# Kernel optimization log

Hardware: AMD Instinct MI355X
Metric: run time of the kernel (lower is better)

## Reference

```python
import jax, jax.numpy as jnp
import numpy as np

B, T, E, H = 8, 2048, 1024, 64

def setup_inputs() -> dict:
    key = jax.random.key(0)
    ks = jax.random.split(key, 7)
    s = 1.0 / np.sqrt(E)
    return {
        "x": jax.random.normal(ks[0], (B, T, E), dtype=jnp.float32),
        "Wq": jax.random.uniform(ks[1], (E, H), jnp.float32, -s, s),
        "bq": jax.random.uniform(ks[2], (H,), jnp.float32, -s, s),
        "Wk": jax.random.uniform(ks[3], (E, H), jnp.float32, -s, s),
        "bk": jax.random.uniform(ks[4], (H,), jnp.float32, -s, s),
        "Wv": jax.random.uniform(ks[5], (E, H), jnp.float32, -s, s),
        "bv": jax.random.uniform(ks[6], (H,), jnp.float32, -s, s),
        "mask": jnp.ones((B, T), dtype=jnp.int32),
    }

def reference(x, Wq, bq, Wk, bk, Wv, bv, mask):
    # QKV projections: [B,T,E] @ [E,H] -> [B,T,H]
    q = x @ Wq + bq
    k = x @ Wk + bk
    v = x @ Wv + bv
    scale = jnp.asarray(H, x.dtype) ** -0.5
    attn = jnp.einsum("bqh,bkh->bqk", q, k) * scale  # [B,T,T]
    pad = mask.astype(bool)[:, None, :]  # key padding mask broadcast over queries
    attn = jnp.where(pad, attn, jnp.asarray(-1e9, attn.dtype))
    attn = jax.nn.softmax(attn, axis=-1)
    # dropout p=0.0 (eval) -> identity
    return jnp.einsum("bqk,bkh->bqh", attn, v)
```

## Files before the change

kernel.cpp:

```cpp
#include <hip/hip_runtime.h>
#include <hip/hip_bf16.h>
#include <stdint.h>


typedef __attribute__((ext_vector_type(8))) short short8;
typedef __attribute__((ext_vector_type(4))) float floatx4;
typedef __attribute__((ext_vector_type(2))) uint32_t uint2v;
typedef __attribute__((ext_vector_type(4))) uint32_t uint4v;

static constexpr int Tn = 2048, En = 1024, Hn = 64;
static constexpr float kLog2e = 1.44269504088896340736f;

static __device__ __forceinline__ ushort f2bf(float f) {
  uint32_t u = __builtin_bit_cast(uint32_t, f);
  u += 0x7FFFu + ((u >> 16) & 1u);
  return (ushort)(u >> 16);
}
static __device__ __forceinline__ uint32_t cvt_pk(float lo, float hi) {
  uint32_t r;
  asm("v_cvt_pk_bf16_f32 %0, %1, %2" : "=v"(r) : "v"(lo), "v"(hi));
  return r;
}

__global__ __launch_bounds__(64) void k_packw(const float* __restrict__ Wq,
                                              const float* __restrict__ Wk,
                                              const float* __restrict__ Wv,
                                              ushort* __restrict__ wpack) {
  int blk = blockIdx.x;
  int kstep = blk / 12, ntile = blk % 12;
  int l = threadIdx.x;
  const float* W = (ntile < 4) ? Wq : (ntile < 8) ? Wk : Wv;
  int col = (ntile & 3) * 16 + (l & 15);
  int k0 = kstep * 32 + (l >> 4) * 8;
  short8 v;
#pragma unroll
  for (int j = 0; j < 8; ++j) v[j] = (short)f2bf(W[(k0 + j) * Hn + col]);
  *reinterpret_cast<short8*>(wpack + ((size_t)(kstep * 12 + ntile) * 64 + l) * 8) = v;
}

__global__ __launch_bounds__(256) void k_qkv(const float* __restrict__ x,
                                             const ushort* __restrict__ wpack,
                                             const float* __restrict__ bq,
                                             const float* __restrict__ bk,
                                             const float* __restrict__ bv,
                                             ushort* __restrict__ q,
                                             ushort* __restrict__ k,
                                             ushort* __restrict__ vT2) {
  __shared__ ushort xs[16][1032];
  int tid = threadIdx.x;
  int batch = blockIdx.x & 7;
  int chunk = blockIdx.x >> 3;
  int row0 = batch * Tn + chunk * 16;

  {
    const float* src = x + (size_t)row0 * En + tid * 4;
#pragma unroll
    for (int i = 0; i < 16; ++i) {
      floatx4 f = *reinterpret_cast<const floatx4*>(src + (size_t)i * En);
      uint2v u;
      u[0] = cvt_pk(f[0], f[1]);
      u[1] = cvt_pk(f[2], f[3]);
      *reinterpret_cast<uint2v*>(&xs[i][tid * 4]) = u;
    }
  }
  __syncthreads();

  int l = tid & 63;
  int w = tid >> 6;
  int lq = l & 15, g = l >> 4;
  const ushort* wpn = wpack + (((size_t)w * 3) * 64 + l) * 8;

  floatx4 acc[3];
#pragma unroll
  for (int nn = 0; nn < 3; ++nn) acc[nn] = (floatx4){0.f, 0.f, 0.f, 0.f};

#pragma unroll 4
  for (int ks = 0; ks < 32; ++ks) {
    short8 af = *reinterpret_cast<const short8*>(&xs[lq][ks * 32 + g * 8]);
#pragma unroll
    for (int nn = 0; nn < 3; ++nn) {
      short8 bf = *reinterpret_cast<const short8*>(wpn + (size_t)ks * 6144 + nn * 512);
      acc[nn] = __builtin_amdgcn_mfma_f32_16x16x32_bf16(af, bf, acc[nn], 0, 0, 0);
    }
  }

#pragma unroll
  for (int nn = 0; nn < 3; ++nn) {
    int n = w * 3 + nn;
    int mat = n >> 2;
    int h = (n & 3) * 16 + lq;
    const float* bias = (mat == 0) ? bq : (mat == 1) ? bk : bv;
    float bias_f = bias[h];
    if (mat == 0) {
#pragma unroll
      for (int r = 0; r < 4; ++r)
        q[(size_t)(row0 + g * 4 + r) * Hn + h] = f2bf((acc[nn][r] + bias_f) * 0.125f);
    } else if (mat == 1) {
#pragma unroll
      for (int r = 0; r < 4; ++r)
        k[(size_t)(row0 + g * 4 + r) * Hn + h] = f2bf(acc[nn][r] + bias_f);
    } else {
      int tile = chunk >> 1;
      int off = (chunk & 1) * 16 + g * 4;
      uint2v pk;
      pk[0] = cvt_pk(acc[nn][0] + bias_f, acc[nn][1] + bias_f);
      pk[1] = cvt_pk(acc[nn][2] + bias_f, acc[nn][3] + bias_f);
      *reinterpret_cast<uint2v*>(vT2 + (((size_t)batch * 64 + tile) * 64 + h) * 32 + off) = pk;
    }
  }
}

__global__ __launch_bounds__(512, 4) void k_attn(const ushort* __restrict__ qm,
                                                 const ushort* __restrict__ km,
                                                 const ushort* __restrict__ vT2,
                                                 const int* __restrict__ mask,
                                                 float* __restrict__ out) {
  __shared__ union SMem {
    ushort P[8][32 * 40];
    struct {
      float accS[4][64][36];
      float mS[4][2][64];
      float lS[4][2][64];
    } mg;
  } sm;

  int tid = threadIdx.x;
  int l = tid & 63, w = tid >> 6;
  int s = w;
  int bid = blockIdx.x;
  int b = bid & 7;
  int chunk = bid >> 3;
  int q0 = chunk * 32;
  int lq = l & 15, g = l >> 4;

  short8 qf[2][2];
#pragma unroll
  for (int qt2 = 0; qt2 < 2; ++qt2) {
    const ushort* qb = qm + ((size_t)(b * Tn + q0 + qt2 * 16 + lq)) * Hn + g * 8;
    qf[qt2][0] = *reinterpret_cast<const short8*>(qb);
    qf[qt2][1] = *reinterpret_cast<const short8*>(qb + 32);
  }

  const ushort* kp = km + ((size_t)(b * Tn + s * 256) + lq) * Hn + g * 8;
  const ushort* vp = vT2 + (((size_t)b * 64 + s * 8) * 64 + lq) * 32 + g * 8;

  const int* mrow = mask + b * Tn + s * 256 + l;
  unsigned long long bal64[4];
#pragma unroll
  for (int j = 0; j < 4; ++j) bal64[j] = __ballot(mrow[j * 64] != 0);

  ushort* Pw = &sm.P[w][0];
  uint32_t* Pw32 = reinterpret_cast<uint32_t*>(Pw);

  float m[2] = {-1e30f, -1e30f};
  float lsum[2] = {0.f, 0.f};
  floatx4 acc[2][4];
#pragma unroll
  for (int qt2 = 0; qt2 < 2; ++qt2)
#pragma unroll
    for (int mt = 0; mt < 4; ++mt) acc[qt2][mt] = (floatx4){0.f, 0.f, 0.f, 0.f};

  short8 kf[2][4];
#pragma unroll
  for (int t = 0; t < 2; ++t)
#pragma unroll
    for (int h = 0; h < 2; ++h)
      kf[0][t * 2 + h] = *reinterpret_cast<const short8*>(kp + t * 1024 + h * 32);

#pragma unroll
  for (int it = 0; it < 8; ++it) {
    const int cur = it & 1, nxt = cur ^ 1;
    if (it < 7) {
#pragma unroll
      for (int t = 0; t < 2; ++t)
#pragma unroll
        for (int h = 0; h < 2; ++h)
          kf[nxt][t * 2 + h] =
              *reinterpret_cast<const short8*>(kp + (it + 1) * 2048 + t * 1024 + h * 32);
    }
    short8 vf[4];
#pragma unroll
    for (int mt = 0; mt < 4; ++mt)
      vf[mt] = *reinterpret_cast<const short8*>(vp + it * 2048 + mt * 512);

    float sc[2][2][4];
#pragma unroll
    for (int qt2 = 0; qt2 < 2; ++qt2)
#pragma unroll
      for (int t = 0; t < 2; ++t) {
        floatx4 z = (floatx4){0.f, 0.f, 0.f, 0.f};
        z = __builtin_amdgcn_mfma_f32_16x16x32_bf16(kf[cur][t * 2 + 0], qf[qt2][0], z, 0, 0, 0);
        z = __builtin_amdgcn_mfma_f32_16x16x32_bf16(kf[cur][t * 2 + 1], qf[qt2][1], z, 0, 0, 0);
#pragma unroll
        for (int r = 0; r < 4; ++r) sc[qt2][t][r] = z[r];
      }
    unsigned int bal32 = (unsigned int)(bal64[it >> 1] >> ((it & 1) * 32));
    if (bal32 != 0xFFFFFFFFu) {
#pragma unroll
      for (int qt2 = 0; qt2 < 2; ++qt2)
#pragma unroll
        for (int t = 0; t < 2; ++t)
#pragma unroll
          for (int r = 0; r < 4; ++r)
            if (!((bal32 >> (t * 16 + g * 4 + r)) & 1u)) sc[qt2][t][r] = -1e9f;
    }
    float pmax0 = fmaxf(fmaxf(fmaxf(sc[0][0][0], sc[0][0][1]), fmaxf(sc[0][0][2], sc[0][0][3])),
                        fmaxf(fmaxf(sc[0][1][0], sc[0][1][1]), fmaxf(sc[0][1][2], sc[0][1][3])));
    float pmax1 = fmaxf(fmaxf(fmaxf(sc[1][0][0], sc[1][0][1]), fmaxf(sc[1][0][2], sc[1][0][3])),
                        fmaxf(fmaxf(sc[1][1][0], sc[1][1][1]), fmaxf(sc[1][1][2], sc[1][1][3])));
    if (!__all((pmax0 - m[0] <= 8.0f) && (pmax1 - m[1] <= 8.0f))) {
      float rm0 = fmaxf(pmax0, __shfl_xor(pmax0, 16));
      rm0 = fmaxf(rm0, __shfl_xor(rm0, 32));
      float rm1 = fmaxf(pmax1, __shfl_xor(pmax1, 16));
      rm1 = fmaxf(rm1, __shfl_xor(rm1, 32));
      float mn0 = fmaxf(m[0], rm0), mn1 = fmaxf(m[1], rm1);
      float a0 = __builtin_amdgcn_exp2f((m[0] - mn0) * kLog2e);
      float a1 = __builtin_amdgcn_exp2f((m[1] - mn1) * kLog2e);
      lsum[0] *= a0; lsum[1] *= a1;
#pragma unroll
      for (int mt = 0; mt < 4; ++mt) { acc[0][mt] *= a0; acc[1][mt] *= a1; }
      m[0] = mn0; m[1] = mn1;
    }
#pragma unroll
    for (int qt2 = 0; qt2 < 2; ++qt2) {
      float nmk = m[qt2] * kLog2e;
      float p[8];
#pragma unroll
      for (int t = 0; t < 2; ++t)
#pragma unroll
        for (int r = 0; r < 4; ++r)
          p[t * 4 + r] = __builtin_amdgcn_exp2f(__builtin_fmaf(sc[qt2][t][r], kLog2e, -nmk));
      lsum[qt2] += ((p[0] + p[1]) + (p[2] + p[3])) + ((p[4] + p[5]) + (p[6] + p[7]));
      uint2v pw0, pw1;
      pw0[0] = cvt_pk(p[0], p[1]); pw0[1] = cvt_pk(p[2], p[3]);
      pw1[0] = cvt_pk(p[4], p[5]); pw1[1] = cvt_pk(p[6], p[7]);
      int row = qt2 * 16 + lq;
      *reinterpret_cast<uint2v*>(Pw32 + row * 20 + g * 2) = pw0;
      *reinterpret_cast<uint2v*>(Pw32 + row * 20 + 8 + g * 2) = pw1;
    }
    short8 pf0 = *reinterpret_cast<const short8*>(Pw + (0 * 16 + lq) * 40 + g * 8);
    short8 pf1 = *reinterpret_cast<const short8*>(Pw + (1 * 16 + lq) * 40 + g * 8);
#pragma unroll
    for (int mt = 0; mt < 4; ++mt) {
      acc[0][mt] = __builtin_amdgcn_mfma_f32_16x16x32_bf16(vf[mt], pf0, acc[0][mt], 0, 0, 0);
      acc[1][mt] = __builtin_amdgcn_mfma_f32_16x16x32_bf16(vf[mt], pf1, acc[1][mt], 0, 0, 0);
    }
  }

#pragma unroll
  for (int qt2 = 0; qt2 < 2; ++qt2) {
    lsum[qt2] += __shfl_xor(lsum[qt2], 16);
    lsum[qt2] += __shfl_xor(lsum[qt2], 32);
  }

  __syncthreads();
  if (s >= 4) {
#pragma unroll
    for (int qt2 = 0; qt2 < 2; ++qt2) {
#pragma unroll
      for (int mt = 0; mt < 4; ++mt)
        *reinterpret_cast<floatx4*>(&sm.mg.accS[s - 4][l][qt2 * 16 + mt * 4]) = acc[qt2][mt];
      sm.mg.mS[s - 4][qt2][l] = m[qt2];
      sm.mg.lS[s - 4][qt2][l] = lsum[qt2];
    }
  }
  __syncthreads();
  if (s < 4) {
#pragma unroll
    for (int qt2 = 0; qt2 < 2; ++qt2) {
      float m2 = sm.mg.mS[s][qt2][l], l2 = sm.mg.lS[s][qt2][l];
      float mn = fmaxf(m[qt2], m2);
      float ea = __builtin_amdgcn_exp2f((m[qt2] - mn) * kLog2e);
      float eb = __builtin_amdgcn_exp2f((m2 - mn) * kLog2e);
      lsum[qt2] = lsum[qt2] * ea + l2 * eb;
#pragma unroll
      for (int mt = 0; mt < 4; ++mt) {
        floatx4 a = *reinterpret_cast<const floatx4*>(&sm.mg.accS[s][l][qt2 * 16 + mt * 4]);
#pragma unroll
        for (int r = 0; r < 4; ++r) acc[qt2][mt][r] = acc[qt2][mt][r] * ea + a[r] * eb;
      }
      m[qt2] = mn;
    }
  }
  __syncthreads();
  if (s >= 1 && s < 4) {
#pragma unroll
    for (int qt2 = 0; qt2 < 2; ++qt2) {
#pragma unroll
      for (int mt = 0; mt < 4; ++mt)
        *reinterpret_cast<floatx4*>(&sm.mg.accS[s - 1][l][qt2 * 16 + mt * 4]) = acc[qt2][mt];
      sm.mg.mS[s - 1][qt2][l] = m[qt2];
      sm.mg.lS[s - 1][qt2][l] = lsum[qt2];
    }
  }
  __syncthreads();
  if (s == 0) {
#pragma unroll
    for (int qt2 = 0; qt2 < 2; ++qt2) {
      float mtot = m[qt2];
#pragma unroll
      for (int si = 0; si < 3; ++si) mtot = fmaxf(mtot, sm.mg.mS[si][qt2][l]);
      float e0 = __builtin_amdgcn_exp2f((m[qt2] - mtot) * kLog2e);
      float ltot = lsum[qt2] * e0;
      float res[4][4];
#pragma unroll
      for (int mt = 0; mt < 4; ++mt)
#pragma unroll
        for (int r = 0; r < 4; ++r) res[mt][r] = acc[qt2][mt][r] * e0;
#pragma unroll
      for (int si = 0; si < 3; ++si) {
        float e = __builtin_amdgcn_exp2f((sm.mg.mS[si][qt2][l] - mtot) * kLog2e);
        ltot += sm.mg.lS[si][qt2][l] * e;
#pragma unroll
        for (int mt = 0; mt < 4; ++mt) {
          floatx4 a = *reinterpret_cast<const floatx4*>(&sm.mg.accS[si][l][qt2 * 16 + mt * 4]);
#pragma unroll
          for (int r = 0; r < 4; ++r) res[mt][r] += a[r] * e;
        }
      }
      float inv = 1.0f / ltot;
      float* obase = out + ((size_t)(b * Tn + q0 + qt2 * 16 + lq)) * Hn;
#pragma unroll
      for (int mt = 0; mt < 4; ++mt) {
        floatx4 o;
#pragma unroll
        for (int r = 0; r < 4; ++r) o[r] = res[mt][r] * inv;
        *reinterpret_cast<floatx4*>(obase + mt * 16 + g * 4) = o;
      }
    }
  }
}

extern "C" void kernel_launch(void* const* d_in, const int* in_sizes, int n_in,
                              void* d_out, int out_size, void* d_ws, size_t ws_size,
                              hipStream_t stream) {
  const float* x  = (const float*)d_in[0];
  const float* Wq = (const float*)d_in[1];
  const float* bq = (const float*)d_in[2];
  const float* Wk = (const float*)d_in[3];
  const float* bk = (const float*)d_in[4];
  const float* Wv = (const float*)d_in[5];
  const float* bv = (const float*)d_in[6];
  const int* mask = (const int*)d_in[7];
  float* outp = (float*)d_out;

  ushort* wpack = (ushort*)d_ws;
  ushort* qbuf  = wpack + 196608;
  ushort* kbuf  = qbuf + (size_t)16384 * 64;
  ushort* vT2   = kbuf + (size_t)16384 * 64;

  hipLaunchKernelGGL(k_packw, dim3(384), dim3(64), 0, stream, Wq, Wk, Wv, wpack);
  hipLaunchKernelGGL(k_qkv, dim3(1024), dim3(256), 0, stream, x, wpack, bq, bk, bv,
                     qbuf, kbuf, vT2);
  hipLaunchKernelGGL(k_attn, dim3(512), dim3(512), 0, stream, qbuf, kbuf, vT2, mask, outp);
}
```

Measured before the change: 65.03 us.

## Restructure QKV projection so each wave owns 16 rows and all 12 output tiles

```diff
diff --git a/kernel.cpp b/kernel.cpp
--- a/kernel.cpp
+++ b/kernel.cpp
@@ -46,47 +46,46 @@
                                              ushort* __restrict__ q,
                                              ushort* __restrict__ k,
                                              ushort* __restrict__ vT2) {
-  __shared__ ushort xs[16][1032];
-  int tid = threadIdx.x;
+  int l = threadIdx.x & 63;
+  int w = threadIdx.x >> 6;
   int batch = blockIdx.x & 7;
   int chunk = blockIdx.x >> 3;
-  int row0 = batch * Tn + chunk * 16;
-
-  {
-    const float* src = x + (size_t)row0 * En + tid * 4;
-#pragma unroll
-    for (int i = 0; i < 16; ++i) {
-      floatx4 f = *reinterpret_cast<const floatx4*>(src + (size_t)i * En);
-      uint2v u;
-      u[0] = cvt_pk(f[0], f[1]);
-      u[1] = cvt_pk(f[2], f[3]);
-      *reinterpret_cast<uint2v*>(&xs[i][tid * 4]) = u;
-    }
-  }
-  __syncthreads();
-
-  int l = tid & 63;
-  int w = tid >> 6;
+  int rl = chunk * 64 + w * 16;
+  int row0 = batch * Tn + rl;
   int lq = l & 15, g = l >> 4;
-  const ushort* wpn = wpack + (((size_t)w * 3) * 64 + l) * 8;
-
-  floatx4 acc[3];
-#pragma unroll
-  for (int nn = 0; nn < 3; ++nn) acc[nn] = (floatx4){0.f, 0.f, 0.f, 0.f};
-
-#pragma unroll 4
+  const float* xrow = x + (size_t)(row0 + lq) * En + g * 8;
+  const ushort* wp = wpack + (size_t)l * 8;
+  floatx4 acc[12];
+#pragma unroll
+  for (int n = 0; n < 12; ++n) acc[n] = (floatx4){0.f, 0.f, 0.f, 0.f};
+
+  floatx4 xa[2][2];
+  xa[0][0] = *reinterpret_cast<const floatx4*>(xrow);
+  xa[0][1] = *reinterpret_cast<const floatx4*>(xrow + 4);
+
   for (int ks = 0; ks < 32; ++ks) {
-    short8 af = *reinterpret_cast<const short8*>(&xs[lq][ks * 32 + g * 8]);
-#pragma unroll
-    for (int nn = 0; nn < 3; ++nn) {
-      short8 bf = *reinterpret_cast<const short8*>(wpn + (size_t)ks * 6144 + nn * 512);
-      acc[nn] = __builtin_amdgcn_mfma_f32_16x16x32_bf16(af, bf, acc[nn], 0, 0, 0);
-    }
-  }
-
-#pragma unroll
-  for (int nn = 0; nn < 3; ++nn) {
-    int n = w * 3 + nn;
+    const int cur = ks & 1, nxt = cur ^ 1;
+    if (ks < 31) {
+      xa[nxt][0] = *reinterpret_cast<const floatx4*>(xrow + (ks + 1) * 32);
+      xa[nxt][1] = *reinterpret_cast<const floatx4*>(xrow + (ks + 1) * 32 + 4);
+    }
+    uint4v aw;
+    aw[0] = cvt_pk(xa[cur][0][0], xa[cur][0][1]);
+    aw[1] = cvt_pk(xa[cur][0][2], xa[cur][0][3]);
+    aw[2] = cvt_pk(xa[cur][1][0], xa[cur][1][1]);
+    aw[3] = cvt_pk(xa[cur][1][2], xa[cur][1][3]);
+    short8 af = __builtin_bit_cast(short8, aw);
+#pragma unroll
+    for (int n = 0; n < 12; ++n) {
+      short8 bf = *reinterpret_cast<const short8*>(wp + (size_t)(ks * 12 + n) * 512);
+      acc[n] = __builtin_amdgcn_mfma_f32_16x16x32_bf16(af, bf, acc[n], 0, 0, 0);
+    }
+  }
+
+  int tile = rl >> 5;
+  int off = ((rl >> 4) & 1) * 16 + g * 4;
+#pragma unroll
+  for (int n = 0; n < 12; ++n) {
     int mat = n >> 2;
     int h = (n & 3) * 16 + lq;
     const float* bias = (mat == 0) ? bq : (mat == 1) ? bk : bv;
@@ -94,17 +93,15 @@
     if (mat == 0) {
 #pragma unroll
       for (int r = 0; r < 4; ++r)
-        q[(size_t)(row0 + g * 4 + r) * Hn + h] = f2bf((acc[nn][r] + bias_f) * 0.125f);
+        q[(size_t)(row0 + g * 4 + r) * Hn + h] = f2bf((acc[n][r] + bias_f) * 0.125f);
     } else if (mat == 1) {
 #pragma unroll
       for (int r = 0; r < 4; ++r)
-        k[(size_t)(row0 + g * 4 + r) * Hn + h] = f2bf(acc[nn][r] + bias_f);
+        k[(size_t)(row0 + g * 4 + r) * Hn + h] = f2bf(acc[n][r] + bias_f);
     } else {
-      int tile = chunk >> 1;
-      int off = (chunk & 1) * 16 + g * 4;
       uint2v pk;
-      pk[0] = cvt_pk(acc[nn][0] + bias_f, acc[nn][1] + bias_f);
-      pk[1] = cvt_pk(acc[nn][2] + bias_f, acc[nn][3] + bias_f);
+      pk[0] = cvt_pk(acc[n][0] + bias_f, acc[n][1] + bias_f);
+      pk[1] = cvt_pk(acc[n][2] + bias_f, acc[n][3] + bias_f);
       *reinterpret_cast<uint2v*>(vT2 + (((size_t)batch * 64 + tile) * 64 + h) * 32 + off) = pk;
     }
   }
@@ -350,7 +347,7 @@
   ushort* vT2   = kbuf + (size_t)16384 * 64;
 
   hipLaunchKernelGGL(k_packw, dim3(384), dim3(64), 0, stream, Wq, Wk, Wv, wpack);
-  hipLaunchKernelGGL(k_qkv, dim3(1024), dim3(256), 0, stream, x, wpack, bq, bk, bv,
+  hipLaunchKernelGGL(k_qkv, dim3(256), dim3(256), 0, stream, x, wpack, bq, bk, bv,
                      qbuf, kbuf, vT2);
   hipLaunchKernelGGL(k_attn, dim3(512), dim3(512), 0, stream, qbuf, kbuf, vT2, mask, outp);
 }
```

After: 70.15 us. 7.9% more time.

## Stream x and weights into LDS with async global_load_lds triple buffering

Applied to the files above, without the earlier changes.

```diff
diff --git a/kernel.cpp b/kernel.cpp
--- a/kernel.cpp
+++ b/kernel.cpp
@@ -20,6 +20,11 @@
   uint32_t r;
   asm("v_cvt_pk_bf16_f32 %0, %1, %2" : "=v"(r) : "v"(lo), "v"(hi));
   return r;
+}
+static __device__ __forceinline__ void gl_lds16(const void* g, void* l) {
+  __builtin_amdgcn_global_load_lds(
+      (const __attribute__((address_space(1))) uint32_t*)g,
+      (__attribute__((address_space(3))) uint32_t*)l, 16, 0, 0);
 }
 
 __global__ __launch_bounds__(64) void k_packw(const float* __restrict__ Wq,
@@ -38,51 +43,77 @@
   *reinterpret_cast<short8*>(wpack + ((size_t)(kstep * 12 + ntile) * 64 + l) * 8) = v;
 }
 
-__global__ __launch_bounds__(256) void k_qkv(const float* __restrict__ x,
-                                             const ushort* __restrict__ wpack,
-                                             const float* __restrict__ bq,
-                                             const float* __restrict__ bk,
-                                             const float* __restrict__ bv,
-                                             ushort* __restrict__ q,
-                                             ushort* __restrict__ k,
-                                             ushort* __restrict__ vT2) {
-  __shared__ ushort xs[16][1032];
+__global__ __launch_bounds__(256, 2) void k_qkv(const float* __restrict__ x,
+                                                const ushort* __restrict__ wpack,
+                                                const float* __restrict__ bq,
+                                                const float* __restrict__ bk,
+                                                const float* __restrict__ bv,
+                                                ushort* __restrict__ q,
+                                                ushort* __restrict__ k,
+                                                ushort* __restrict__ vT2) {
+  __shared__ float lx[4][3][512];
+  __shared__ ushort lw[4][3][3][512];
+
   int tid = threadIdx.x;
+  int l = tid & 63;
+  int w = tid >> 6;
   int batch = blockIdx.x & 7;
   int chunk = blockIdx.x >> 3;
   int row0 = batch * Tn + chunk * 16;
-
-  {
-    const float* src = x + (size_t)row0 * En + tid * 4;
-#pragma unroll
-    for (int i = 0; i < 16; ++i) {
-      floatx4 f = *reinterpret_cast<const floatx4*>(src + (size_t)i * En);
-      uint2v u;
-      u[0] = cvt_pk(f[0], f[1]);
-      u[1] = cvt_pk(f[2], f[3]);
-      *reinterpret_cast<uint2v*>(&xs[i][tid * 4]) = u;
-    }
-  }
-  __syncthreads();
-
-  int l = tid & 63;
-  int w = tid >> 6;
   int lq = l & 15, g = l >> 4;
-  const ushort* wpn = wpack + (((size_t)w * 3) * 64 + l) * 8;
+
+  int srow = l >> 3;
+  int sslot = (l & 7) ^ (srow & 7);
+  const float* xg0 = x + (size_t)(row0 + srow) * En + sslot * 4;
+  const float* xg1 = x + (size_t)(row0 + 8 + srow) * En + sslot * 4;
+  const ushort* wg = wpack + ((size_t)(w * 3) * 64 + l) * 8;
+
+#define ISSUE_SET(J)                                                          \
+  {                                                                           \
+    const int bf_ = (J) % 3;                                                  \
+    gl_lds16(xg0 + (J) * 32, &lx[w][bf_][0]);                                 \
+    gl_lds16(xg1 + (J) * 32, &lx[w][bf_][256]);                               \
+    gl_lds16(wg + (size_t)((J) * 12 + 0) * 512, &lw[w][bf_][0][0]);           \
+    gl_lds16(wg + (size_t)((J) * 12 + 1) * 512, &lw[w][bf_][1][0]);           \
+    gl_lds16(wg + (size_t)((J) * 12 + 2) * 512, &lw[w][bf_][2][0]);           \
+  }
 
   floatx4 acc[3];
 #pragma unroll
-  for (int nn = 0; nn < 3; ++nn) acc[nn] = (floatx4){0.f, 0.f, 0.f, 0.f};
-
-#pragma unroll 4
-  for (int ks = 0; ks < 32; ++ks) {
-    short8 af = *reinterpret_cast<const short8*>(&xs[lq][ks * 32 + g * 8]);
+  for (int n = 0; n < 3; ++n) acc[n] = (floatx4){0.f, 0.f, 0.f, 0.f};
+
+  ISSUE_SET(0)
+  ISSUE_SET(1)
+
+#pragma unroll
+  for (int j = 0; j < 32; ++j) {
+    if (j < 31) {
+      asm volatile("s_waitcnt vmcnt(5)" ::: "memory");
+    } else {
+      asm volatile("s_waitcnt vmcnt(0)" ::: "memory");
+    }
+    __builtin_amdgcn_sched_barrier(0);
+
+    const int bf = j % 3;
+    floatx4 x0 = *reinterpret_cast<const floatx4*>(
+        &lx[w][bf][lq * 32 + (((g * 2 + 0) ^ (lq & 7)) << 2)]);
+    floatx4 x1 = *reinterpret_cast<const floatx4*>(
+        &lx[w][bf][lq * 32 + (((g * 2 + 1) ^ (lq & 7)) << 2)]);
+    uint4v aw;
+    aw[0] = cvt_pk(x0[0], x0[1]);
+    aw[1] = cvt_pk(x0[2], x0[3]);
+    aw[2] = cvt_pk(x1[0], x1[1]);
+    aw[3] = cvt_pk(x1[2], x1[3]);
+    short8 af = __builtin_bit_cast(short8, aw);
 #pragma unroll
     for (int nn = 0; nn < 3; ++nn) {
-      short8 bf = *reinterpret_cast<const short8*>(wpn + (size_t)ks * 6144 + nn * 512);
-      acc[nn] = __builtin_amdgcn_mfma_f32_16x16x32_bf16(af, bf, acc[nn], 0, 0, 0);
-    }
-  }
+      short8 bfh = *reinterpret_cast<const short8*>(&lw[w][bf][nn][l * 8]);
+      acc[nn] = __builtin_amdgcn_mfma_f32_16x16x32_bf16(af, bfh, acc[nn], 0, 0, 0);
+    }
+    __builtin_amdgcn_sched_barrier(0);
+    if (j + 2 < 32) ISSUE_SET(j + 2)
+  }
+#undef ISSUE_SET
 
 #pragma unroll
   for (int nn = 0; nn < 3; ++nn) {
```

Measured after the change: 66.99 us. +3.0%, slower.
